# Kernel optimization log

Hardware: AMD Instinct MI355X
Metric: run time of the kernel (lower is better)

## Reference

```python
import jax, jax.numpy as jnp
import numpy as np

B, C, H, W = 4, 256, 64, 64
CI = 3
TEMPERATURE = 0.0001 * 5
EPS = 2.220446049250313e-16  # sys.float_info.epsilon


def _nearest_up4(x):
    # nn.Upsample(scale_factor=4, mode='nearest'): [B,C,H,W] -> [B,C,4H,4W]
    return jnp.repeat(jnp.repeat(x, 4, axis=2), 4, axis=3)


def _avg_pool2(x):
    # AvgPool2d(kernel=2, stride=2, pad=0)
    b, c, h, w = x.shape
    return x.reshape(b, c, h // 2, 2, w // 2, 2).mean(axis=(3, 5))


def _center_norm(feats):
    # subtract per-channel spatial mean, then L2-normalize over channels per position
    b, c, h, w = feats.shape
    t = feats.reshape(b, c, h * w)
    t = t - t.mean(axis=-1, keepdims=True)
    n = jnp.linalg.norm(t, axis=1, keepdims=True) + EPS
    return t / n  # [B,C,HW]


def setup_inputs() -> dict:
    key = jax.random.key(0)
    k1, k2, k3 = jax.random.split(key, 3)
    return {
        "x_feats": jax.random.normal(k1, (B, C, H, W), jnp.float32),
        "y_feats": jax.random.normal(k2, (B, C, H, W), jnp.float32),
        "y_img": jax.random.uniform(k3, (B, CI, 4 * H, 4 * W), jnp.float32),
    }


def reference(x_feats, y_feats, y_img):
    b, c, h, w = x_feats.shape
    hw = h * w
    theta = _center_norm(x_feats)  # [B,C,HW]
    phi = _center_norm(y_feats)    # [B,C,HW]
    f = jnp.einsum('bcm,bcn->bmn', theta, phi)  # dense correlation [B,HW,HW]
    loss_feat_pair = jnp.mean(jnp.abs(theta - phi))  # F.l1_loss(theta, phi)
    # WTA_scale_weight == 1 -> WTA branch bypassed, just temperature scaling
    f_wta = f / TEMPERATURE
    f_div_c = jax.nn.softmax(f_wta, axis=-1)  # [B,HW,HW]
    # warped features: f_div_C @ y_feats^T
    b_lab = y_feats.reshape(b, c, hw)
    y = jnp.einsum('bmn,bcn->bcm', f_div_c, b_lab).reshape(b, c, h, w)
    # soft-argmax coordinates
    xc = (jnp.arange(hw) % w).astype(x_feats.dtype)   # [HW]
    yc = (jnp.arange(hw) // w).astype(x_feats.dtype)  # [HW]
    coords_x = f_div_c @ xc  # [B,HW]
    coords_y = f_div_c @ yc  # [B,HW]
    coords1 = jnp.stack([coords_x, coords_y], axis=1).reshape(b, 2, h, w)
    coords0 = jnp.stack([xc, yc], axis=0).reshape(1, 2, h, w)
    flow = _nearest_up4(coords1 - coords0)  # [B,2,4H,4W]
    # image warping branch (y_img is not None)
    yi = _avg_pool2(_avg_pool2(y_img))  # [B,CI,H,W]
    ci = yi.shape[1]
    yi_flat = yi.reshape(b, ci, hw)
    y_img_attn = jnp.einsum('bmn,bcn->bmc', f_div_c, yi_flat)  # [B,HW,CI]
    f_div_c_v = jax.nn.softmax(jnp.swapaxes(f_wta, 1, 2), axis=-1)
    y_img_cyc = jnp.einsum('bmn,bnc->bcm', f_div_c_v, y_img_attn).reshape(b, ci, h, w)
    y_img_out = jnp.swapaxes(y_img_attn, 1, 2).reshape(b, ci, h, w)
    return (y, flow, _nearest_up4(y_img_out), _nearest_up4(y_img_cyc), loss_feat_pair)
```

## Files before the change

### kernel.cpp

```cpp
#include <hip/hip_runtime.h>
#include <math.h>

#define HW   4096
#define NCH  256
#define NB   4

constexpr float TEMP  = (float)(0.0001 * 5.0);
constexpr float INV_T = 1.0f / TEMP;
constexpr float EPSN  = 2.220446049250313e-16f;

typedef __attribute__((ext_vector_type(8))) _Float16 f16x8;
typedef __attribute__((ext_vector_type(4))) _Float16 f16x4;
typedef __attribute__((ext_vector_type(4))) float    f32x4;

constexpr size_t OFF_YT    = 0;
constexpr size_t OFF_YI    = OFF_YT    + (size_t)NB*HW*NCH;
constexpr size_t OFF_MEAN  = OFF_YI    + (size_t)NB*3*HW;
constexpr size_t OFF_RNORM = OFF_MEAN  + (size_t)2*NB*NCH;
constexpr size_t OFF_NSQP  = OFF_RNORM + (size_t)2*NB*HW;
constexpr size_t OFF_F     = OFF_NSQP  + (size_t)2*NB*8*HW;
constexpr size_t OFF_YP    = OFF_F     + (size_t)HW*HW;
constexpr size_t OFF_ROWP  = OFF_YP;
constexpr size_t OFF_COLP  = OFF_YP + (size_t)32*7*HW;
constexpr size_t OFF_RMAX  = OFF_YP    + (size_t)8*NCH*HW;
constexpr size_t OFF_RSUM  = OFF_RMAX  + HW;
constexpr size_t OFF_CMAX  = OFF_RSUM  + HW;
constexpr size_t OFF_COORD = OFF_CMAX  + HW;
constexpr size_t OFF_ATTN  = OFF_COORD + (size_t)NB*2*HW;
constexpr size_t OFF_CYC   = OFF_ATTN  + (size_t)NB*HW*3;
constexpr size_t OFF_CYCP  = OFF_CYC   + (size_t)NB*3*HW;
constexpr size_t OFF_LOSSP = OFF_CYCP  + (size_t)32*4*HW;
constexpr size_t OFF_F16   = OFF_LOSSP + 1024;

constexpr size_t OUT_Y    = 0;
constexpr size_t OUT_FLOW = (size_t)NB*NCH*HW;
constexpr size_t OUT_IMG  = OUT_FLOW + (size_t)NB*2*256*256;
constexpr size_t OUT_CYCO = OUT_IMG  + (size_t)NB*3*256*256;
constexpr size_t OUT_LOSS = OUT_CYCO + (size_t)NB*3*256*256;

__device__ __forceinline__ void gload16(const void* g, void* l) {
    __builtin_amdgcn_global_load_lds(
        (const __attribute__((address_space(1))) unsigned int*)g,
        (__attribute__((address_space(3))) unsigned int*)l, 16, 0, 0);
}

__global__ void mean_kernel(const float* __restrict__ xf, const float* __restrict__ yf,
                            float* __restrict__ means) {
    const float* src = (blockIdx.y == 0 ? xf : yf) + (size_t)blockIdx.x * HW;
    float s = 0.f;
    for (int i = threadIdx.x; i < HW; i += 256) s += src[i];
    __shared__ float red[256];
    red[threadIdx.x] = s; __syncthreads();
    for (int st = 128; st > 0; st >>= 1) {
        if (threadIdx.x < st) red[threadIdx.x] += red[threadIdx.x + st];
        __syncthreads();
    }
    if (threadIdx.x == 0) means[blockIdx.y * (NB*NCH) + blockIdx.x] = red[0] * (1.0f / HW);
}

__global__ void nsq_combine_kernel(const float* __restrict__ part, float* __restrict__ rnorms,
                                   int b) {
    int t = blockIdx.y;
    int m = blockIdx.x * 256 + threadIdx.x;
    const float* p = part + ((size_t)t*NB + b) * 8 * HW + m;
    float s = 0.f;
    for (int k = 0; k < 8; ++k) s += p[(size_t)k * HW];
    rnorms[((size_t)t*NB + b) * HW + m] = 1.0f / (sqrtf(s) + EPSN);
}

__global__ void ycast_kernel(const float* __restrict__ yf, _Float16* __restrict__ yf16) {
    size_t i = ((size_t)blockIdx.x * 256 + threadIdx.x) * 8;
    const float4* s = (const float4*)(yf + i);
    float4 v0 = s[0], v1 = s[1];
    f16x8 o;
    o[0]=(_Float16)v0.x; o[1]=(_Float16)v0.y; o[2]=(_Float16)v0.z; o[3]=(_Float16)v0.w;
    o[4]=(_Float16)v1.x; o[5]=(_Float16)v1.y; o[6]=(_Float16)v1.z; o[7]=(_Float16)v1.w;
    *(f16x8*)(yf16 + i) = o;
}

__global__ void prep_kernel(const float* __restrict__ xf, const float* __restrict__ yf,
                            const float* __restrict__ means,
                            _Float16* __restrict__ th, _Float16* __restrict__ tl,
                            _Float16* __restrict__ ph, _Float16* __restrict__ pl,
                            float* __restrict__ nsqp, int b) {
    __shared__ float tile[32][33];
    __shared__ float sqr[8][33];
    int t = blockIdx.z;
    int c0 = blockIdx.x * 32, m0 = blockIdx.y * 32;
    const float* src = (t == 0 ? xf : yf) + (size_t)b * NCH * HW;
    const float* mn  = means + t * (NB*NCH) + b * NCH;
    int tx = threadIdx.x & 31, ty = threadIdx.x >> 5;
    float sq = 0.f;
    for (int i = ty; i < 32; i += 8) {
        float v = src[(size_t)(c0 + i) * HW + m0 + tx] - mn[c0 + i];
        tile[i][tx] = v;
        sq += v * v;
    }
    sqr[ty][tx] = sq;
    __syncthreads();
    _Float16* H = (t == 0 ? th : ph);
    _Float16* L = (t == 0 ? tl : pl);
    for (int i = ty; i < 32; i += 8) {
        float v = tile[tx][i];
        _Float16 h = (_Float16)v;
        _Float16 l = (_Float16)(v - (float)h);
        H[(size_t)(m0 + i)*NCH + c0 + tx] = h;
        L[(size_t)(m0 + i)*NCH + c0 + tx] = l;
    }
    if (ty == 0) {
        float s = 0.f;
        #pragma unroll
        for (int k = 0; k < 8; ++k) s += sqr[k][tx];
        nsqp[(((size_t)t*NB + b) * 8 + blockIdx.x) * HW + m0 + tx] = s;
    }
}

__global__ void avgpool_kernel(const float* __restrict__ yimg, float* __restrict__ yi) {
    size_t idx = (size_t)blockIdx.x * 256 + threadIdx.x;
    int m  = (int)(idx & (HW - 1));
    int bc = (int)(idx >> 12);
    int h = m >> 6, w = m & 63;
    const float* p = yimg + (size_t)bc * 65536 + (size_t)(h*4) * 256 + w*4;
    float s = 0.f;
    #pragma unroll
    for (int dy = 0; dy < 4; ++dy) {
        #pragma unroll
        for (int dx = 0; dx < 4; ++dx) s += p[dy*256 + dx];
    }
    yi[idx] = s * (1.0f/16.0f);
}

__global__ __launch_bounds__(512) void gemm_f_kernel(
        const _Float16* __restrict__ th, const _Float16* __restrict__ tl,
        const _Float16* __restrict__ ph, const _Float16* __restrict__ pl,
        const float* __restrict__ rnorms, const float* __restrict__ yi,
        float* __restrict__ f, float* __restrict__ rowp, float* __restrict__ colp,
        int b) {
    __shared__ char lds[2][4][8192];
    int tid  = threadIdx.x;
    int lane = tid & 63;
    int w = tid >> 6;
    int wm = w >> 2;
    int wn = w & 3;
    int m0 = blockIdx.y * 128, n0 = blockIdx.x * 128;

    int o0 = tid * 16;
    int r0 = o0 >> 6, s0 = (o0 >> 4) & 3, g0 = s0 ^ ((r0 >> 1) & 3);
    size_t ga0 = (size_t)(n0 + r0)*NCH + g0*8;
    size_t gb0 = (size_t)(m0 + r0)*NCH + g0*8;

    int fra = wm*64 + (lane & 15);
    int frb = wn*32 + (lane & 15);
    int ks  = lane >> 4;

    auto STAGE = [&](int buf, int k0) {
        gload16(ph + ga0 + k0, &lds[buf][0][o0]);
        gload16(pl + ga0 + k0, &lds[buf][1][o0]);
        gload16(th + gb0 + k0, &lds[buf][2][o0]);
        gload16(tl + gb0 + k0, &lds[buf][3][o0]);
    };

    f32x4 acc[4][2];
    #pragma unroll
    for (int i = 0; i < 4; ++i)
        #pragma unroll
        for (int j = 0; j < 2; ++j) acc[i][j] = (f32x4){0.f, 0.f, 0.f, 0.f};

    STAGE(0, 0);
    __syncthreads();
    int cur = 0;
    for (int kt = 0; kt < 8; ++kt) {
        if (kt < 7) STAGE(cur ^ 1, (kt + 1) * 32);

        f16x8 ah[4], al[4], bh[2], bl[2];
        #pragma unroll
        for (int i = 0; i < 4; ++i) {
            int rowa = fra + i*16;
            int offa = rowa*64 + ((ks ^ ((rowa >> 1) & 3)) << 4);
            ah[i] = *(const f16x8*)&lds[cur][0][offa];
            al[i] = *(const f16x8*)&lds[cur][1][offa];
        }
        #pragma unroll
        for (int j = 0; j < 2; ++j) {
            int rowb = frb + j*16;
            int offb = rowb*64 + ((ks ^ ((rowb >> 1) & 3)) << 4);
            bh[j] = *(const f16x8*)&lds[cur][2][offb];
            bl[j] = *(const f16x8*)&lds[cur][3][offb];
        }
        __builtin_amdgcn_s_setprio(1);
        #pragma unroll
        for (int i = 0; i < 4; ++i)
            #pragma unroll
            for (int j = 0; j < 2; ++j) {
                acc[i][j] = __builtin_amdgcn_mfma_f32_16x16x32_f16(ah[i], bh[j], acc[i][j], 0, 0, 0);
                acc[i][j] = __builtin_amdgcn_mfma_f32_16x16x32_f16(ah[i], bl[j], acc[i][j], 0, 0, 0);
                acc[i][j] = __builtin_amdgcn_mfma_f32_16x16x32_f16(al[i], bh[j], acc[i][j], 0, 0, 0);
            }
        __builtin_amdgcn_s_setprio(0);
        __syncthreads();
        cur ^= 1;
    }

    const float* rnx = rnorms + (size_t)b * HW;
    const float* rny = rnorms + (size_t)(NB + b) * HW;
    int mg[2];  float rxv[2];
    #pragma unroll
    for (int j = 0; j < 2; ++j) {
        mg[j] = m0 + wn*32 + j*16 + (lane & 15);
        rxv[j] = rnx[mg[j]];
    }
    int nl0 = wm*64 + (lane >> 4)*4;
    #pragma unroll
    for (int i = 0; i < 4; ++i)
        #pragma unroll
        for (int r = 0; r < 4; ++r) {
            float ry = rny[n0 + nl0 + i*16 + r];
            #pragma unroll
            for (int j = 0; j < 2; ++j) acc[i][j][r] *= rxv[j] * ry;
        }

    #pragma unroll
    for (int j = 0; j < 2; ++j)
        #pragma unroll
        for (int i = 0; i < 4; ++i)
            *(f32x4*)&f[(size_t)mg[j]*HW + n0 + nl0 + i*16] = acc[i][j];

    float* S     = (float*)&lds[0][0][0];
    float* rowm  = S;
    float* sums6 = S + 256;
    float* colm  = S + 1792;

    #pragma unroll
    for (int j = 0; j < 2; ++j) {
        float v = acc[0][j][0];
        #pragma unroll
        for (int i = 0; i < 4; ++i)
            #pragma unroll
            for (int r = 0; r < 4; ++r) v = fmaxf(v, acc[i][j][r]);
        v = fmaxf(v, __shfl_xor(v, 16));
        v = fmaxf(v, __shfl_xor(v, 32));
        if (lane < 16) rowm[wm*128 + wn*32 + j*16 + lane] = v;
    }
    #pragma unroll
    for (int i = 0; i < 4; ++i)
        #pragma unroll
        for (int r = 0; r < 4; ++r) {
            float v = fmaxf(acc[i][0][r], acc[i][1][r]);
            #pragma unroll
            for (int d = 1; d < 16; d <<= 1) v = fmaxf(v, __shfl_xor(v, d));
            if ((lane & 15) == 0) colm[wn*128 + nl0 + i*16 + r] = v;
        }
    __syncthreads();

    float bm[2];
    #pragma unroll
    for (int j = 0; j < 2; ++j) {
        int ml = wn*32 + j*16 + (lane & 15);
        bm[j] = fmaxf(rowm[ml], rowm[128 + ml]);
    }
    float a6[2][6];
    #pragma unroll
    for (int j = 0; j < 2; ++j)
        #pragma unroll
        for (int q = 0; q < 6; ++q) a6[j][q] = 0.f;
    const float* yib = yi + (size_t)b * 3 * HW;
    #pragma unroll
    for (int i = 0; i < 4; ++i)
        #pragma unroll
        for (int r = 0; r < 4; ++r) {
            int ng = n0 + nl0 + i*16 + r;
            float xc = (float)(ng & 63), yc = (float)(ng >> 6);
            float y0 = yib[ng], y1 = yib[HW + ng], y2 = yib[2*HW + ng];
            #pragma unroll
            for (int j = 0; j < 2; ++j) {
                float e = __expf((acc[i][j][r] - bm[j]) * INV_T);
                a6[j][0] += e;      a6[j][1] += e*xc; a6[j][2] += e*yc;
                a6[j][3] += e*y0;   a6[j][4] += e*y1; a6[j][5] += e*y2;
            }
        }
    #pragma unroll
    for (int j = 0; j < 2; ++j)
        #pragma unroll
        for (int q = 0; q < 6; ++q) {
            float v = a6[j][q];
            v += __shfl_xor(v, 16);
            v += __shfl_xor(v, 32);
            if (lane < 16) sums6[(wm*128 + wn*32 + j*16 + lane)*6 + q] = v;
        }
    __syncthreads();

    if (tid < 128) {
        int ml = tid;
        float m2 = fmaxf(rowm[ml], rowm[128 + ml]);
        rowp[((size_t)blockIdx.x*7 + 0)*HW + m0 + ml] = m2;
        #pragma unroll
        for (int q = 0; q < 6; ++q)
            rowp[((size_t)blockIdx.x*7 + 1 + q)*HW + m0 + ml] =
                sums6[ml*6 + q] + sums6[(128 + ml)*6 + q];
    } else if (tid < 256) {
        int nl = tid - 128;
        float c2 = fmaxf(fmaxf(colm[nl], colm[128 + nl]),
                         fmaxf(colm[256 + nl], colm[384 + nl]));
        colp[(size_t)blockIdx.y*HW + n0 + nl] = c2;
    }
}

__global__ void rowcol_combine_kernel(const float* __restrict__ rowp,
        const float* __restrict__ colp,
        float* __restrict__ rmax, float* __restrict__ rsuminv,
        float* __restrict__ coords, float* __restrict__ attn,
        float* __restrict__ cmax, int b) {
    int idx = blockIdx.x * 256 + threadIdx.x;
    if (blockIdx.y == 0) {
        int m = idx;
        float gm = -3.0e38f;
        for (int t = 0; t < 32; ++t) gm = fmaxf(gm, rowp[((size_t)t*7)*HW + m]);
        float S=0, CX=0, CY=0, A0=0, A1=0, A2=0;
        for (int t = 0; t < 32; ++t) {
            const float* p = rowp + (size_t)t*7*HW + m;
            float wgt = __expf((p[0] - gm) * INV_T);
            S  += p[1*HW] * wgt; CX += p[2*HW] * wgt; CY += p[3*HW] * wgt;
            A0 += p[4*HW] * wgt; A1 += p[5*HW] * wgt; A2 += p[6*HW] * wgt;
        }
        float inv = 1.0f / S;
        rmax[m] = gm; rsuminv[m] = inv;
        coords[((size_t)b*2 + 0)*HW + m] = CX * inv;
        coords[((size_t)b*2 + 1)*HW + m] = CY * inv;
        attn[((size_t)b*HW + m)*3 + 0] = A0 * inv;
        attn[((size_t)b*HW + m)*3 + 1] = A1 * inv;
        attn[((size_t)b*HW + m)*3 + 2] = A2 * inv;
    } else {
        int n = idx;
        float gm = -3.0e38f;
        for (int t = 0; t < 32; ++t) gm = fmaxf(gm, colp[(size_t)t*HW + n]);
        cmax[n] = gm;
    }
}

__global__ __launch_bounds__(512) void gemm_y_kernel(const float* __restrict__ f,
        const float* __restrict__ rmax, const _Float16* __restrict__ yf16,
        _Float16* __restrict__ yph, int b) {
    __shared__ __align__(16) char ldsA[4096];
    __shared__ __align__(16) char ldsB[16384];
    int tid  = threadIdx.x;
    int lane = tid & 63;
    int w = tid >> 6, wm = w >> 2, wn = w & 3;
    int m0 = blockIdx.x * 64;
    int ks = blockIdx.y;
    const _Float16* Yb = yf16 + (size_t)b * NCH * HW;

    int ar = tid >> 3, kc = tid & 7;
    int aslot = kc >> 1, ahalf = kc & 1;
    int aoff = ar*64 + ((aslot ^ ((ar >> 1) & 3)) << 4) + ahalf*8;
    float arm = rmax[m0 + ar];
    const float* frow = f + (size_t)(m0 + ar)*HW + kc*4;

    int o0 = tid*16, o1 = o0 + 8192;
    int br0 = o0 >> 6, bs0 = (o0 >> 4) & 3, bg0 = bs0 ^ ((br0 >> 1) & 3);
    int br1 = o1 >> 6, bs1 = (o1 >> 4) & 3, bg1 = bs1 ^ ((br1 >> 1) & 3);
    size_t gb0 = (size_t)br0*HW + bg0*8;
    size_t gb1 = (size_t)br1*HW + bg1*8;

    int fra = wm*32 + (lane & 15);
    int frb = wn*64 + (lane & 15);
    int kslot = lane >> 4;

    f32x4 acc[2][4];
    #pragma unroll
    for (int i = 0; i < 2; ++i)
        #pragma unroll
        for (int j = 0; j < 4; ++j) acc[i][j] = (f32x4){0.f, 0.f, 0.f, 0.f};

    for (int k0 = ks*1024; k0 < ks*1024 + 1024; k0 += 32) {
        gload16(Yb + gb0 + k0, &ldsB[o0]);
        gload16(Yb + gb1 + k0, &ldsB[o1]);
        {
            float4 v = *(const float4*)(frow + k0);
            f16x4 pk;
            pk[0] = (_Float16)__expf((v.x - arm) * INV_T);
            pk[1] = (_Float16)__expf((v.y - arm) * INV_T);
            pk[2] = (_Float16)__expf((v.z - arm) * INV_T);
            pk[3] = (_Float16)__expf((v.w - arm) * INV_T);
            *(f16x4*)&ldsA[aoff] = pk;
        }
        __syncthreads();

        f16x8 af[2], bf[4];
        #pragma unroll
        for (int i = 0; i < 2; ++i) {
            int rowa = fra + i*16;
            af[i] = *(const f16x8*)&ldsA[rowa*64 + ((kslot ^ ((rowa >> 1) & 3)) << 4)];
        }
        #pragma unroll
        for (int j = 0; j < 4; ++j) {
            int rowb = frb + j*16;
            bf[j] = *(const f16x8*)&ldsB[rowb*64 + ((kslot ^ ((rowb >> 1) & 3)) << 4)];
        }
        __builtin_amdgcn_s_setprio(1);
        #pragma unroll
        for (int i = 0; i < 2; ++i)
            #pragma unroll
            for (int j = 0; j < 4; ++j)
                acc[i][j] = __builtin_amdgcn_mfma_f32_16x16x32_f16(af[i], bf[j], acc[i][j], 0, 0, 0);
        __builtin_amdgcn_s_setprio(0);
        __syncthreads();
    }

    #pragma unroll
    for (int i = 0; i < 2; ++i) {
        int m = m0 + wm*32 + i*16 + (lane >> 4) * 4;
        #pragma unroll
        for (int j = 0; j < 4; ++j) {
            int c = wn*64 + j*16 + (lane & 15);
            f16x4 v;
            #pragma unroll
            for (int r = 0; r < 4; ++r) v[r] = (_Float16)acc[i][j][r];
            *(f16x4*)(yph + ((size_t)ks*NCH + c)*HW + m) = v;
        }
    }
}

__global__ void ycombine_kernel(const _Float16* __restrict__ yph, const float* __restrict__ rsuminv,
                                float* __restrict__ out, int b) {
    size_t idx = (size_t)blockIdx.x * 256 + threadIdx.x;
    int m = (int)(idx & (HW - 1));
    float s = 0.f;
    #pragma unroll
    for (int k = 0; k < 4; ++k) s += (float)yph[(size_t)k*NCH*HW + idx];
    out[OUT_Y + (size_t)b*NCH*HW + idx] = s * rsuminv[m];
}

__global__ __launch_bounds__(256) void cyc_partial_kernel(const float* __restrict__ f,
        const float* __restrict__ cmax, const float* __restrict__ attn,
        float* __restrict__ part, int b) {
    __shared__ float at[128*3];
    int i  = blockIdx.x * 256 + threadIdx.x;
    int j0 = blockIdx.y * 128;
    for (int k = threadIdx.x; k < 384; k += 256)
        at[k] = attn[((size_t)b*HW + j0)*3 + k];
    __syncthreads();
    float cm = cmax[i];
    float a0=0, a1=0, a2=0, a3=0;
    for (int jj = 0; jj < 128; ++jj) {
        float e = __expf((f[(size_t)(j0+jj)*HW + i] - cm) * INV_T);
        a0 = fmaf(e, at[jj*3+0], a0);
        a1 = fmaf(e, at[jj*3+1], a1);
        a2 = fmaf(e, at[jj*3+2], a2);
        a3 += e;
    }
    part[((size_t)blockIdx.y*4 + 0)*HW + i] = a0;
    part[((size_t)blockIdx.y*4 + 1)*HW + i] = a1;
    part[((size_t)blockIdx.y*4 + 2)*HW + i] = a2;
    part[((size_t)blockIdx.y*4 + 3)*HW + i] = a3;
}

__global__ void cyc_combine_kernel(const float* __restrict__ part,
                                   float* __restrict__ cyc, int b) {
    int i = blockIdx.x * 256 + threadIdx.x;
    int c = blockIdx.y;
    float s = 0.f, den = 0.f;
    for (int k = 0; k < 32; ++k) {
        s   += part[((size_t)k*4 + c)*HW + i];
        den += part[((size_t)k*4 + 3)*HW + i];
    }
    cyc[((size_t)b*3 + c)*HW + i] = s / den;
}

__global__ void flow_kernel(const float* __restrict__ coords, float* __restrict__ out) {
    size_t idx = (size_t)blockIdx.x * 256 + threadIdx.x;
    int x4 = (int)(idx & 255);
    int y4 = (int)((idx >> 8) & 255);
    int ch = (int)((idx >> 16) & 1);
    int b  = (int)(idx >> 17);
    int w = x4 >> 2, h = y4 >> 2;
    int m = h*64 + w;
    float c1 = coords[((size_t)b*2 + ch)*HW + m];
    float c0 = (ch == 0) ? (float)w : (float)h;
    out[OUT_FLOW + idx] = c1 - c0;
}

__global__ void imgout_kernel(const float* __restrict__ attn, const float* __restrict__ cyc,
                              float* __restrict__ out) {
    size_t idx = (size_t)blockIdx.x * 256 + threadIdx.x;
    int x4 = (int)(idx & 255);
    int y4 = (int)((idx >> 8) & 255);
    int rest = (int)(idx >> 16);
    int ch = rest % 3, b = rest / 3;
    int m = (y4 >> 2)*64 + (x4 >> 2);
    out[OUT_IMG  + idx] = attn[((size_t)b*HW + m)*3 + ch];
    out[OUT_CYCO + idx] = cyc[((size_t)b*3 + ch)*HW + m];
}

__global__ void loss_partial_kernel(const float* __restrict__ xf, const float* __restrict__ yf,
                                    const float* __restrict__ means, const float* __restrict__ rnorms,
                                    float* __restrict__ part) {
    __shared__ float red[256];
    size_t base = (size_t)blockIdx.x * 4096;
    float s = 0.f;
    for (int k = 0; k < 16; ++k) {
        size_t id = base + (size_t)k*256 + threadIdx.x;
        int m  = (int)(id & (HW - 1));
        int bc = (int)(id >> 12);
        int b  = bc >> 8;
        float th = (xf[id] - means[bc])          * rnorms[(size_t)b*HW + m];
        float ph = (yf[id] - means[NB*NCH + bc]) * rnorms[(size_t)(NB + b)*HW + m];
        s += fabsf(th - ph);
    }
    red[threadIdx.x] = s; __syncthreads();
    for (int st = 128; st > 0; st >>= 1) {
        if (threadIdx.x < st) red[threadIdx.x] += red[threadIdx.x + st];
        __syncthreads();
    }
    if (threadIdx.x == 0) part[blockIdx.x] = red[0];
}

__global__ void loss_final_kernel(const float* __restrict__ part, float* __restrict__ out) {
    __shared__ float red[256];
    float s = 0.f;
    for (int k = threadIdx.x; k < 1024; k += 256) s += part[k];
    red[threadIdx.x] = s; __syncthreads();
    for (int st = 128; st > 0; st >>= 1) {
        if (threadIdx.x < st) red[threadIdx.x] += red[threadIdx.x + st];
        __syncthreads();
    }
    if (threadIdx.x == 0) out[OUT_LOSS] = red[0] * (1.0f / 4194304.0f);
}

extern "C" void kernel_launch(void* const* d_in, const int* in_sizes, int n_in,
                              void* d_out, int out_size, void* d_ws, size_t ws_size,
                              hipStream_t stream) {
    (void)in_sizes; (void)n_in; (void)out_size; (void)ws_size;
    const float* xf   = (const float*)d_in[0];
    const float* yf   = (const float*)d_in[1];
    const float* yimg = (const float*)d_in[2];
    float* out = (float*)d_out;
    float* ws  = (float*)d_ws;

    _Float16* yf16 = (_Float16*)(ws + OFF_YT);
    float* yi      = ws + OFF_YI;
    float* means   = ws + OFF_MEAN;
    float* rnorms  = ws + OFF_RNORM;
    float* nsqp    = ws + OFF_NSQP;
    float* fbuf    = ws + OFF_F;
    _Float16* yph  = (_Float16*)(ws + OFF_YP);
    float* rowp    = ws + OFF_ROWP;
    float* colp    = ws + OFF_COLP;
    float* rmax    = ws + OFF_RMAX;
    float* rsuminv = ws + OFF_RSUM;
    float* cmax    = ws + OFF_CMAX;
    float* coords  = ws + OFF_COORD;
    float* attn    = ws + OFF_ATTN;
    float* cyc     = ws + OFF_CYC;
    float* cycp    = ws + OFF_CYCP;
    float* lossp   = ws + OFF_LOSSP;
    _Float16* th = (_Float16*)(ws + OFF_F16);
    _Float16* tl = th + (size_t)HW*NCH;
    _Float16* ph = tl + (size_t)HW*NCH;
    _Float16* pl = ph + (size_t)HW*NCH;

    mean_kernel        <<<dim3(NB*NCH, 2),   256, 0, stream>>>(xf, yf, means);
    ycast_kernel       <<<2048,              256, 0, stream>>>(yf, yf16);
    avgpool_kernel     <<<NB*3*HW/256,       256, 0, stream>>>(yimg, yi);

    for (int b = 0; b < NB; ++b) {
        prep_kernel          <<<dim3(8, 128, 2), 256, 0, stream>>>(xf, yf, means, th, tl, ph, pl,
                                                                   nsqp, b);
        nsq_combine_kernel   <<<dim3(16, 2),     256, 0, stream>>>(nsqp, rnorms, b);
        gemm_f_kernel        <<<dim3(32, 32),    512, 0, stream>>>(th, tl, ph, pl, rnorms, yi,
                                                                   fbuf, rowp, colp, b);
        rowcol_combine_kernel<<<dim3(16, 2),     256, 0, stream>>>(rowp, colp, rmax, rsuminv,
                                                                   coords, attn, cmax, b);
        gemm_y_kernel        <<<dim3(64, 4),     512, 0, stream>>>(fbuf, rmax, yf16, yph, b);
        ycombine_kernel      <<<NCH*HW/256,      256, 0, stream>>>(yph, rsuminv, out, b);
        cyc_partial_kernel   <<<dim3(16, 32),    256, 0, stream>>>(fbuf, cmax, attn, cycp, b);
        cyc_combine_kernel   <<<dim3(16, 3),     256, 0, stream>>>(cycp, cyc, b);
    }

    flow_kernel        <<<NB*2*65536/256, 256, 0, stream>>>(coords, out);
    imgout_kernel      <<<NB*3*65536/256, 256, 0, stream>>>(attn, cyc, out);
    loss_partial_kernel<<<1024,           256, 0, stream>>>(xf, yf, means, rnorms, lossp);
    loss_final_kernel  <<<1,              256, 0, stream>>>(lossp, out);
}
```

Baseline: 515.9 us.

## Store block-relative scaled logits as fp16 instead of fp32 correlation matrix

The GEMM kernel no longer writes the fp32 correlation matrix. It writes fp16 logits shifted by each 128-column block's local row max, plus those per-block row maxima. The downstream softmax-GEMM and cyclic kernels read the fp16 buffer and rebuild exponentials with a per-block correction factor. This halves the write and read traffic of the 64 MB-per-batch F matrix. The cost is fp16 rounding of logits that can reach large magnitudes (scaled by 1/0.0005), which can cost accuracy in the exponent, especially for the column softmax.

```diff
diff --git a/kernel.cpp b/kernel.cpp
--- a/kernel.cpp
+++ b/kernel.cpp
@@ -25,7 +25,8 @@
 constexpr size_t OFF_RMAX  = OFF_YP    + (size_t)8*NCH*HW;
 constexpr size_t OFF_RSUM  = OFF_RMAX  + HW;
 constexpr size_t OFF_CMAX  = OFF_RSUM  + HW;
-constexpr size_t OFF_COORD = OFF_CMAX  + HW;
+constexpr size_t OFF_RMB   = OFF_CMAX  + HW;
+constexpr size_t OFF_COORD = OFF_RMB   + (size_t)32*HW;
 constexpr size_t OFF_ATTN  = OFF_COORD + (size_t)NB*2*HW;
 constexpr size_t OFF_CYC   = OFF_ATTN  + (size_t)NB*HW*3;
 constexpr size_t OFF_CYCP  = OFF_CYC   + (size_t)NB*3*HW;
@@ -134,8 +135,8 @@
         const _Float16* __restrict__ th, const _Float16* __restrict__ tl,
         const _Float16* __restrict__ ph, const _Float16* __restrict__ pl,
         const float* __restrict__ rnorms, const float* __restrict__ yi,
-        float* __restrict__ f, float* __restrict__ rowp, float* __restrict__ colp,
-        int b) {
+        _Float16* __restrict__ zh, float* __restrict__ rowp, float* __restrict__ colp,
+        float* __restrict__ rmb, int b) {
     __shared__ char lds[2][4][8192];
     int tid  = threadIdx.x;
     int lane = tid & 63;
@@ -219,12 +220,6 @@
             for (int j = 0; j < 2; ++j) acc[i][j][r] *= rxv[j] * ry;
         }
 
-    #pragma unroll
-    for (int j = 0; j < 2; ++j)
-        #pragma unroll
-        for (int i = 0; i < 4; ++i)
-            *(f32x4*)&f[(size_t)mg[j]*HW + n0 + nl0 + i*16] = acc[i][j];
-
     float* S     = (float*)&lds[0][0][0];
     float* rowm  = S;
     float* sums6 = S + 256;
@@ -265,7 +260,8 @@
         for (int q = 0; q < 6; ++q) a6[j][q] = 0.f;
     const float* yib = yi + (size_t)b * 3 * HW;
     #pragma unroll
-    for (int i = 0; i < 4; ++i)
+    for (int i = 0; i < 4; ++i) {
+        f16x4 zq[2];
         #pragma unroll
         for (int r = 0; r < 4; ++r) {
             int ng = n0 + nl0 + i*16 + r;
@@ -273,11 +269,17 @@
             float y0 = yib[ng], y1 = yib[HW + ng], y2 = yib[2*HW + ng];
             #pragma unroll
             for (int j = 0; j < 2; ++j) {
-                float e = __expf((acc[i][j][r] - bm[j]) * INV_T);
+                float z = (acc[i][j][r] - bm[j]) * INV_T;
+                float e = __expf(z);
+                zq[j][r] = (_Float16)z;
                 a6[j][0] += e;      a6[j][1] += e*xc; a6[j][2] += e*yc;
                 a6[j][3] += e*y0;   a6[j][4] += e*y1; a6[j][5] += e*y2;
             }
         }
+        #pragma unroll
+        for (int j = 0; j < 2; ++j)
+            *(f16x4*)&zh[(size_t)mg[j]*HW + n0 + nl0 + i*16] = zq[j];
+    }
     #pragma unroll
     for (int j = 0; j < 2; ++j)
         #pragma unroll
@@ -293,6 +295,7 @@
         int ml = tid;
         float m2 = fmaxf(rowm[ml], rowm[128 + ml]);
         rowp[((size_t)blockIdx.x*7 + 0)*HW + m0 + ml] = m2;
+        rmb[(size_t)blockIdx.x*HW + m0 + ml] = m2;
         #pragma unroll
         for (int q = 0; q < 6; ++q)
             rowp[((size_t)blockIdx.x*7 + 1 + q)*HW + m0 + ml] =
@@ -337,9 +340,9 @@
     }
 }
 
-__global__ __launch_bounds__(512) void gemm_y_kernel(const float* __restrict__ f,
-        const float* __restrict__ rmax, const _Float16* __restrict__ yf16,
-        _Float16* __restrict__ yph, int b) {
+__global__ __launch_bounds__(512) void gemm_y_kernel(const _Float16* __restrict__ zh,
+        const float* __restrict__ rmax, const float* __restrict__ rmb,
+        const _Float16* __restrict__ yf16, _Float16* __restrict__ yph, int b) {
     __shared__ __align__(16) char ldsA[4096];
     __shared__ __align__(16) char ldsB[16384];
     int tid  = threadIdx.x;
@@ -352,8 +355,9 @@
     int ar = tid >> 3, kc = tid & 7;
     int aslot = kc >> 1, ahalf = kc & 1;
     int aoff = ar*64 + ((aslot ^ ((ar >> 1) & 3)) << 4) + ahalf*8;
-    float arm = rmax[m0 + ar];
-    const float* frow = f + (size_t)(m0 + ar)*HW + kc*4;
+    float gm = rmax[m0 + ar];
+    const _Float16* zrow = zh + (size_t)(m0 + ar)*HW + kc*4;
+    const float* rmbm = rmb + (m0 + ar);
 
     int o0 = tid*16, o1 = o0 + 8192;
     int br0 = o0 >> 6, bs0 = (o0 >> 4) & 3, bg0 = bs0 ^ ((br0 >> 1) & 3);
@@ -371,16 +375,19 @@
         #pragma unroll
         for (int j = 0; j < 4; ++j) acc[i][j] = (f32x4){0.f, 0.f, 0.f, 0.f};
 
+    float corrf = 0.f;
     for (int k0 = ks*1024; k0 < ks*1024 + 1024; k0 += 32) {
         gload16(Yb + gb0 + k0, &ldsB[o0]);
         gload16(Yb + gb1 + k0, &ldsB[o1]);
         {
-            float4 v = *(const float4*)(frow + k0);
+            if ((k0 & 127) == 0)
+                corrf = __expf((rmbm[(size_t)(k0 >> 7)*HW] - gm) * INV_T);
+            f16x4 zv = *(const f16x4*)(zrow + k0);
             f16x4 pk;
-            pk[0] = (_Float16)__expf((v.x - arm) * INV_T);
-            pk[1] = (_Float16)__expf((v.y - arm) * INV_T);
-            pk[2] = (_Float16)__expf((v.z - arm) * INV_T);
-            pk[3] = (_Float16)__expf((v.w - arm) * INV_T);
+            pk[0] = (_Float16)(__expf((float)zv[0]) * corrf);
+            pk[1] = (_Float16)(__expf((float)zv[1]) * corrf);
+            pk[2] = (_Float16)(__expf((float)zv[2]) * corrf);
+            pk[3] = (_Float16)(__expf((float)zv[3]) * corrf);
             *(f16x4*)&ldsA[aoff] = pk;
         }
         __syncthreads();
@@ -430,19 +437,26 @@
     out[OUT_Y + (size_t)b*NCH*HW + idx] = s * rsuminv[m];
 }
 
-__global__ __launch_bounds__(256) void cyc_partial_kernel(const float* __restrict__ f,
-        const float* __restrict__ cmax, const float* __restrict__ attn,
-        float* __restrict__ part, int b) {
+__global__ __launch_bounds__(256) void cyc_partial_kernel(const _Float16* __restrict__ zh,
+        const float* __restrict__ cmax, const float* __restrict__ rmb,
+        const float* __restrict__ attn, float* __restrict__ part, int b) {
     __shared__ float at[128*3];
+    __shared__ float bmL[2][128];
     int i  = blockIdx.x * 256 + threadIdx.x;
     int j0 = blockIdx.y * 128;
     for (int k = threadIdx.x; k < 384; k += 256)
         at[k] = attn[((size_t)b*HW + j0)*3 + k];
+    {
+        int k = threadIdx.x;
+        bmL[k >> 7][k & 127] = rmb[((size_t)(blockIdx.x*2 + (k >> 7)))*HW + j0 + (k & 127)];
+    }
     __syncthreads();
     float cm = cmax[i];
+    int tl = threadIdx.x >> 7;
     float a0=0, a1=0, a2=0, a3=0;
     for (int jj = 0; jj < 128; ++jj) {
-        float e = __expf((f[(size_t)(j0+jj)*HW + i] - cm) * INV_T);
+        float z = (float)zh[(size_t)(j0+jj)*HW + i];
+        float e = __expf(z + (bmL[tl][jj] - cm) * INV_T);
         a0 = fmaf(e, at[jj*3+0], a0);
         a1 = fmaf(e, at[jj*3+1], a1);
         a2 = fmaf(e, at[jj*3+2], a2);
@@ -541,13 +555,14 @@
     float* means   = ws + OFF_MEAN;
     float* rnorms  = ws + OFF_RNORM;
     float* nsqp    = ws + OFF_NSQP;
-    float* fbuf    = ws + OFF_F;
+    _Float16* zh   = (_Float16*)(ws + OFF_F);
     _Float16* yph  = (_Float16*)(ws + OFF_YP);
     float* rowp    = ws + OFF_ROWP;
     float* colp    = ws + OFF_COLP;
     float* rmax    = ws + OFF_RMAX;
     float* rsuminv = ws + OFF_RSUM;
     float* cmax    = ws + OFF_CMAX;
+    float* rmb     = ws + OFF_RMB;
     float* coords  = ws + OFF_COORD;
     float* attn    = ws + OFF_ATTN;
     float* cyc     = ws + OFF_CYC;
@@ -567,12 +582,12 @@
                                                                    nsqp, b);
         nsq_combine_kernel   <<<dim3(16, 2),     256, 0, stream>>>(nsqp, rnorms, b);
         gemm_f_kernel        <<<dim3(32, 32),    512, 0, stream>>>(th, tl, ph, pl, rnorms, yi,
-                                                                   fbuf, rowp, colp, b);
+                                                                   zh, rowp, colp, rmb, b);
         rowcol_combine_kernel<<<dim3(16, 2),     256, 0, stream>>>(rowp, colp, rmax, rsuminv,
                                                                    coords, attn, cmax, b);
-        gemm_y_kernel        <<<dim3(64, 4),     512, 0, stream>>>(fbuf, rmax, yf16, yph, b);
+        gemm_y_kernel        <<<dim3(64, 4),     512, 0, stream>>>(zh, rmax, rmb, yf16, yph, b);
         ycombine_kernel      <<<NCH*HW/256,      256, 0, stream>>>(yph, rsuminv, out, b);
-        cyc_partial_kernel   <<<dim3(16, 32),    256, 0, stream>>>(fbuf, cmax, attn, cycp, b);
+        cyc_partial_kernel   <<<dim3(16, 32),    256, 0, stream>>>(zh, cmax, rmb, attn, cycp, b);
         cyc_combine_kernel   <<<dim3(16, 3),     256, 0, stream>>>(cycp, cyc, b);
     }
 
```

New measurement: 503.3 us. 1.03x faster.
